# Kernel optimization log

Hardware: AMD Instinct MI355X
Metric: run time of the kernel (lower is better)

## Reference

```python
import jax, jax.numpy as jnp
import numpy as np

DEGREE = 6
START_DEGREE = 0


def setup_inputs() -> dict:
    key = jax.random.key(0)
    k1, k2 = jax.random.split(key)
    batch, in_features, out_features = 4096, 1024, 1024
    width = DEGREE - START_DEGREE + 1
    x = jax.random.normal(k1, (batch, in_features), dtype=jnp.float32)
    coeffs = jax.random.normal(k2, (out_features, width), dtype=jnp.float32) * 0.1
    sigma = jnp.ones((1,), dtype=jnp.float32)
    return {"x": x, "coeffs": coeffs, "sigma": sigma}


def reference(x, coeffs, sigma):
    # x: (B, F); coeffs: (O, W); sigma: (1,)
    s = jnp.clip(sigma, 0.1, 5.0)
    xs = x / s  # (B, F)
    # Probabilists'-style Hermite recursion (as written in the source module)
    polys = [jnp.ones_like(xs)]
    if DEGREE >= 1:
        polys.append(2.0 * xs)
        for n in range(2, DEGREE + 1):
            Hn = 2.0 * xs * polys[-1] - 2.0 * (n - 1) * polys[-2]
            polys.append(jnp.clip(Hn, -100.0, 100.0))
    P = jnp.stack(polys[START_DEGREE:DEGREE + 1], axis=1)  # (B, W, F)
    gaussian = jnp.exp(-jnp.minimum(xs * xs, 50.0))        # (B, F)
    P = P * gaussian[:, None, :]                           # (B, W, F)
    # Algebraically equivalent to sum over W of coeffs*poly then sum over F:
    # reduce over in_features first, then tiny contraction with coeffs.
    basis = P.sum(axis=-1)                                 # (B, W)
    return jnp.einsum('bw,ow->bo', basis, coeffs)          # (B, O)
```

## Files before the change

kernel.cpp:

```cpp
#include <hip/hip_runtime.h>

#define F_DIM   1024
#define O_DIM   1024
#define W_DIM   7
#define BLOCK   256
#define RB      8

__global__ __launch_bounds__(BLOCK) void hermite_fused(
    const float* __restrict__ x,
    const float* __restrict__ coeffs,
    const float* __restrict__ sigma,
    float* __restrict__ out)
{
    const int tid  = threadIdx.x;
    const int lane = tid & 63;
    const int wave = tid >> 6;
    const int r0   = blockIdx.x * RB + wave * 2;

    const float s     = fminf(fmaxf(sigma[0], 0.1f), 5.0f);
    const float inv_s = 1.0f / s;

    float basis[2][W_DIM];

#pragma unroll
    for (int rr = 0; rr < 2; ++rr) {
        const float4* xrow = (const float4*)(x + (size_t)(r0 + rr) * F_DIM);

        float4 v[4];
        v[0] = xrow[lane];
        v[1] = xrow[lane + 64];
        v[2] = xrow[lane + 128];
        v[3] = xrow[lane + 192];

        float acc[W_DIM];
#pragma unroll
        for (int w = 0; w < W_DIM; ++w) acc[w] = 0.0f;

#pragma unroll
        for (int q = 0; q < 4; ++q) {
            const float el[4] = {v[q].x, v[q].y, v[q].z, v[q].w};
#pragma unroll
            for (int e = 0; e < 4; ++e) {
                const float xs = el[e] * inv_s;
                const float g  = __expf(-fminf(xs * xs, 50.0f));
                float hm2 = 1.0f;
                float hm1 = 2.0f * xs;
                acc[0] += g;
                acc[1] += hm1 * g;
#pragma unroll
                for (int n = 2; n <= 6; ++n) {
                    float hn = 2.0f * xs * hm1 - 2.0f * (float)(n - 1) * hm2;
                    hn = fminf(fmaxf(hn, -100.0f), 100.0f);
                    acc[n] += hn * g;
                    hm2 = hm1;
                    hm1 = hn;
                }
            }
        }

#pragma unroll
        for (int w = 0; w < W_DIM; ++w) {
            float a = acc[w];
#pragma unroll
            for (int m = 32; m > 0; m >>= 1)
                a += __shfl_xor(a, m, 64);
            basis[rr][w] = a;
        }
    }

#pragma unroll
    for (int q = 0; q < 4; ++q) {
        const int k = q * 64 + lane;
        const float4* cp = (const float4*)(coeffs + (size_t)28 * k);
        float cf[28];
#pragma unroll
        for (int j = 0; j < 7; ++j) {
            const float4 c4 = cp[j];
            cf[4 * j + 0] = c4.x; cf[4 * j + 1] = c4.y;
            cf[4 * j + 2] = c4.z; cf[4 * j + 3] = c4.w;
        }

#pragma unroll
        for (int rr = 0; rr < 2; ++rr) {
            float4 a;
            a.x = basis[rr][0] * cf[0];
            a.y = basis[rr][0] * cf[7];
            a.z = basis[rr][0] * cf[14];
            a.w = basis[rr][0] * cf[21];
#pragma unroll
            for (int w = 1; w < W_DIM; ++w) {
                const float bw = basis[rr][w];
                a.x = fmaf(bw, cf[w],      a.x);
                a.y = fmaf(bw, cf[7 + w],  a.y);
                a.z = fmaf(bw, cf[14 + w], a.z);
                a.w = fmaf(bw, cf[21 + w], a.w);
            }
            ((float4*)(out + (size_t)(r0 + rr) * O_DIM))[k] = a;
        }
    }
}

extern "C" void kernel_launch(void* const* d_in, const int* in_sizes, int n_in,
                              void* d_out, int out_size, void* d_ws, size_t ws_size,
                              hipStream_t stream) {
    const float* x      = (const float*)d_in[0];
    const float* coeffs = (const float*)d_in[1];
    const float* sigma  = (const float*)d_in[2];
    float* out          = (float*)d_out;

    const int B = in_sizes[0] / F_DIM;
    hermite_fused<<<dim3(B / RB), dim3(BLOCK), 0, stream>>>(x, coeffs, sigma, out);
}
```

Measured before the change: 78.38 us.

## Stage transposed coeffs in LDS and process one row per wave

Each block cooperatively loads the full coefficient table into shared memory in a transposed layout. The output contraction then reads contiguous float4 per basis term from LDS instead of doing per-thread strided global loads. Rows per block are halved so each wave handles one row, which doubles the grid size. The cost is a 28 KB LDS footprint per block, which limits occupancy, plus redundant coefficient loading in every block and a barrier.

```diff
diff --git a/kernel.cpp b/kernel.cpp
--- a/kernel.cpp
+++ b/kernel.cpp
@@ -4,9 +4,9 @@
 #define O_DIM   1024
 #define W_DIM   7
 #define BLOCK   256
-#define RB      8
+#define RB      4
 
-__global__ __launch_bounds__(BLOCK) void hermite_fused(
+__global__ __launch_bounds__(BLOCK, 4) void hermite_fused(
     const float* __restrict__ x,
     const float* __restrict__ coeffs,
     const float* __restrict__ sigma,
@@ -15,88 +15,93 @@
     const int tid  = threadIdx.x;
     const int lane = tid & 63;
     const int wave = tid >> 6;
-    const int r0   = blockIdx.x * RB + wave * 2;
+    const int row  = blockIdx.x * RB + wave;
+
+    __shared__ float ct[W_DIM][O_DIM];
+
+    const float4* xrow = (const float4*)(x + (size_t)row * F_DIM);
+    float4 v[4];
+    v[0] = xrow[lane];
+    v[1] = xrow[lane + 64];
+    v[2] = xrow[lane + 128];
+    v[3] = xrow[lane + 192];
+
+    {
+        float tmp[28];
+        const float4* cg = (const float4*)coeffs + 7 * tid;
+#pragma unroll
+        for (int j = 0; j < 7; ++j) {
+            const float4 c4 = cg[j];
+            tmp[4 * j + 0] = c4.x; tmp[4 * j + 1] = c4.y;
+            tmp[4 * j + 2] = c4.z; tmp[4 * j + 3] = c4.w;
+        }
+        const int o0 = 4 * tid;
+#pragma unroll
+        for (int i = 0; i < 28; ++i)
+            ct[i % 7][o0 + i / 7] = tmp[i];
+    }
 
     const float s     = fminf(fmaxf(sigma[0], 0.1f), 5.0f);
     const float inv_s = 1.0f / s;
 
-    float basis[2][W_DIM];
+    __syncthreads();
+
+    float acc[W_DIM];
+#pragma unroll
+    for (int w = 0; w < W_DIM; ++w) acc[w] = 0.0f;
 
 #pragma unroll
-    for (int rr = 0; rr < 2; ++rr) {
-        const float4* xrow = (const float4*)(x + (size_t)(r0 + rr) * F_DIM);
-
-        float4 v[4];
-        v[0] = xrow[lane];
-        v[1] = xrow[lane + 64];
-        v[2] = xrow[lane + 128];
-        v[3] = xrow[lane + 192];
-
-        float acc[W_DIM];
+    for (int q = 0; q < 4; ++q) {
+        const float el[4] = {v[q].x, v[q].y, v[q].z, v[q].w};
 #pragma unroll
-        for (int w = 0; w < W_DIM; ++w) acc[w] = 0.0f;
-
+        for (int e = 0; e < 4; ++e) {
+            const float xs = el[e] * inv_s;
+            const float g  = __expf(-fminf(xs * xs, 50.0f));
+            float hm2 = 1.0f;
+            float hm1 = 2.0f * xs;
+            acc[0] += g;
+            acc[1] += hm1 * g;
 #pragma unroll
-        for (int q = 0; q < 4; ++q) {
-            const float el[4] = {v[q].x, v[q].y, v[q].z, v[q].w};
-#pragma unroll
-            for (int e = 0; e < 4; ++e) {
-                const float xs = el[e] * inv_s;
-                const float g  = __expf(-fminf(xs * xs, 50.0f));
-                float hm2 = 1.0f;
-                float hm1 = 2.0f * xs;
-                acc[0] += g;
-                acc[1] += hm1 * g;
-#pragma unroll
-                for (int n = 2; n <= 6; ++n) {
-                    float hn = 2.0f * xs * hm1 - 2.0f * (float)(n - 1) * hm2;
-                    hn = fminf(fmaxf(hn, -100.0f), 100.0f);
-                    acc[n] += hn * g;
-                    hm2 = hm1;
-                    hm1 = hn;
-                }
+            for (int n = 2; n <= 6; ++n) {
+                float hn = 2.0f * xs * hm1 - 2.0f * (float)(n - 1) * hm2;
+                hn = fminf(fmaxf(hn, -100.0f), 100.0f);
+                acc[n] += hn * g;
+                hm2 = hm1;
+                hm1 = hn;
             }
-        }
-
-#pragma unroll
-        for (int w = 0; w < W_DIM; ++w) {
-            float a = acc[w];
-#pragma unroll
-            for (int m = 32; m > 0; m >>= 1)
-                a += __shfl_xor(a, m, 64);
-            basis[rr][w] = a;
         }
     }
 
+    float basis[W_DIM];
+#pragma unroll
+    for (int w = 0; w < W_DIM; ++w) {
+        float a = acc[w];
+#pragma unroll
+        for (int m = 32; m > 0; m >>= 1)
+            a += __shfl_xor(a, m, 64);
+        basis[w] = a;
+    }
+
+    float* orow = out + (size_t)row * O_DIM;
 #pragma unroll
     for (int q = 0; q < 4; ++q) {
         const int k = q * 64 + lane;
-        const float4* cp = (const float4*)(coeffs + (size_t)28 * k);
-        float cf[28];
+        float4 a;
+        {
+            const float4 c = *(const float4*)&ct[0][4 * k];
+            a.x = basis[0] * c.x; a.y = basis[0] * c.y;
+            a.z = basis[0] * c.z; a.w = basis[0] * c.w;
+        }
 #pragma unroll
-        for (int j = 0; j < 7; ++j) {
-            const float4 c4 = cp[j];
-            cf[4 * j + 0] = c4.x; cf[4 * j + 1] = c4.y;
-            cf[4 * j + 2] = c4.z; cf[4 * j + 3] = c4.w;
+        for (int w = 1; w < W_DIM; ++w) {
+            const float4 c  = *(const float4*)&ct[w][4 * k];
+            const float bw = basis[w];
+            a.x = fmaf(bw, c.x, a.x);
+            a.y = fmaf(bw, c.y, a.y);
+            a.z = fmaf(bw, c.z, a.z);
+            a.w = fmaf(bw, c.w, a.w);
         }
-
-#pragma unroll
-        for (int rr = 0; rr < 2; ++rr) {
-            float4 a;
-            a.x = basis[rr][0] * cf[0];
-            a.y = basis[rr][0] * cf[7];
-            a.z = basis[rr][0] * cf[14];
-            a.w = basis[rr][0] * cf[21];
-#pragma unroll
-            for (int w = 1; w < W_DIM; ++w) {
-                const float bw = basis[rr][w];
-                a.x = fmaf(bw, cf[w],      a.x);
-                a.y = fmaf(bw, cf[7 + w],  a.y);
-                a.z = fmaf(bw, cf[14 + w], a.z);
-                a.w = fmaf(bw, cf[21 + w], a.w);
-            }
-            ((float4*)(out + (size_t)(r0 + rr) * O_DIM))[k] = a;
-        }
+        ((float4*)orow)[k] = a;
     }
 }
 
```

Measured after the change: 73.90 us. -5.7%, faster.
